# Performance work log

Hardware: AMD Instinct MI355X
Metric: run time of the kernel (lower is better)

## Reference

```python
import jax, jax.numpy as jnp
from jax import lax
import numpy as np

NF = 64   # nf
T = 7     # in_nc == 2*radius+1 frames
KS = 3    # deform kernel size
K = KS * KS


def conv2d(x, w, b, stride=1, pad=1):
    out = lax.conv_general_dilated(x, w, (stride, stride), [(pad, pad), (pad, pad)],
                                   dimension_numbers=('NCHW', 'OIHW', 'NCHW'))
    return out + b[None, :, None, None]


def convT2d(x, w, b):
    # torch ConvTranspose2d(k=4, stride=2, padding=1); w: (Cin, Cout, 4, 4)
    wf = jnp.flip(w, (2, 3)).transpose(1, 0, 2, 3)
    out = lax.conv_general_dilated(x, wf, (1, 1), [(2, 2), (2, 2)], lhs_dilation=(2, 2),
                                   dimension_numbers=('NCHW', 'OIHW', 'NCHW'))
    return out + b[None, :, None, None]


def bilinear_gather(img, ys, xs):
    # img: (C, H, W); ys/xs: (...,) absolute pixel coords; zero padding outside
    C, H, W = img.shape
    y0 = jnp.floor(ys); x0 = jnp.floor(xs)
    wy = ys - y0; wx = xs - x0

    def tap(yi, xi, wgt):
        valid = (yi >= 0) & (yi <= H - 1) & (xi >= 0) & (xi <= W - 1)
        yc = jnp.clip(yi, 0, H - 1).astype(jnp.int32)
        xc = jnp.clip(xi, 0, W - 1).astype(jnp.int32)
        return img[:, yc, xc] * (wgt * valid.astype(img.dtype))

    return (tap(y0, x0, (1 - wy) * (1 - wx)) + tap(y0, x0 + 1, (1 - wy) * wx)
            + tap(y0 + 1, x0, wy * (1 - wx)) + tap(y0 + 1, x0 + 1, wy * wx))


def flow_warp(x, flow):
    # x: (C, H, W); flow: (H, W, 2) with (dx, dy); align_corners=True grid_sample
    # with the normalization in the torch code reduces to absolute-pixel bilinear.
    H, W = x.shape[-2:]
    gy, gx = jnp.meshgrid(jnp.arange(H, dtype=x.dtype), jnp.arange(W, dtype=x.dtype), indexing='ij')
    return bilinear_gather(x, gy + flow[..., 1], gx + flow[..., 0])


def mod_deform_conv(x, off, msk, w, b):
    # Modulated deformable conv v2; deformable_groups = Cin (1 channel per group).
    B, Cin, H, W = x.shape
    G = Cin
    off = off.reshape(B, G, K, 2, H, W)   # per-group (dy, dx) per kernel tap
    msk = msk.reshape(B, G, K, H, W)
    gy, gx = jnp.meshgrid(jnp.arange(H, dtype=x.dtype), jnp.arange(W, dtype=x.dtype), indexing='ij')
    kk = jnp.arange(K)
    ky = (kk // KS - KS // 2).astype(x.dtype)
    kx = (kk % KS - KS // 2).astype(x.dtype)
    ys = gy[None, None, None] + ky[None, None, :, None, None] + off[:, :, :, 0]  # (B,G,K,H,W)
    xs = gx[None, None, None] + kx[None, None, :, None, None] + off[:, :, :, 1]
    xg = x.reshape(B, G, 1, H, W)
    samp = jax.vmap(jax.vmap(jax.vmap(bilinear_gather, in_axes=(None, 0, 0)),
                             in_axes=(0, 0, 0)), in_axes=(0, 0, 0))(xg, ys, xs)
    # samp: (B, G, K, 1, H, W)
    mod = samp * msk[:, :, :, None]
    wk = w.reshape(w.shape[0], G, 1, K)   # (O, G, Cpg=1, K)
    out = jnp.einsum('bgkchw,ogck->bohw', mod, wk)
    return out + b[None, :, None, None]


def _agg(feats, aligned, pred, ff_w, ff_b, dn1_w, dn1_b, dn2_w, dn2_b,
         tr_cw, tr_cb, tr_tw, tr_tb, up1_cw, up1_cb, up1_tw, up1_tb,
         up2_cw, up2_cb, up2_tw, up2_tb):
    B, T_, C, H, W = feats.shape
    ref = feats[:, T_ // 2][:, None]                      # center frame embedding
    p1 = jax.nn.sigmoid(aligned * ref)
    p2 = jax.nn.sigmoid(pred * ref)
    a1 = (aligned * p1).reshape(B, T_ * C, H, W)
    a2 = (pred * p2).reshape(B, T_ * C, H, W)
    f = feats.reshape(B, T_ * C, H, W)
    fuse = lambda z: jax.nn.leaky_relu(conv2d(z, ff_w, ff_b), 0.1)
    out0 = 0.1 * fuse(a1 + a2) + fuse(f)
    out1 = jax.nn.relu(conv2d(out0, dn1_w, dn1_b, stride=2))
    out2 = jax.nn.relu(conv2d(out1, dn2_w, dn2_b, stride=2))
    out = jax.nn.relu(convT2d(jax.nn.relu(conv2d(out2, tr_cw, tr_cb, stride=2)), tr_tw, tr_tb))
    out = jax.nn.relu(convT2d(jax.nn.relu(conv2d(jnp.concatenate([out, out2], 1), up2_cw, up2_cb)), up2_tw, up2_tb))
    out = jax.nn.relu(convT2d(jax.nn.relu(conv2d(jnp.concatenate([out, out1], 1), up1_cw, up1_cb)), up1_tw, up1_tb))
    return out


def _forward(lqs, preds, mv, bw1, bb1, bw2, bb2, dn1_w, dn1_b, dn2_w, dn2_b,
             up1_cw, up1_cb, up1_tw, up1_tb, up2_cw, up2_cb, up2_tw, up2_tb,
             tr_cw, tr_cb, tr_tw, tr_tb, ff_w, ff_b, om_w, om_b, dc_w, dc_b):
    B, T_, H, W = lqs.shape
    bb = lambda z: conv2d(conv2d(z, bw1, bb1), bw2, bb2)
    feat = bb(lqs.reshape(B * T_, 1, H, W)).reshape(B, T_, NF, H, W)
    pred_feat = bb(preds).reshape(B, T_, NF, H, W)
    # alg_MV_fea[:,0] = feat[:,0]; alg_MV_fea[:,i] = warp(feat[:,i-1], mv[:,i-1])
    prev = feat[:, :T_ - 1].reshape(B * (T_ - 1), NF, H, W)
    flows = mv.reshape(B * (T_ - 1), H, W, 2)
    warped = jax.vmap(flow_warp)(prev, flows).reshape(B, T_ - 1, NF, H, W)
    alg = jnp.concatenate([feat[:, :1], warped], axis=1)
    feat_f = _agg(feat, alg, pred_feat, ff_w, ff_b, dn1_w, dn1_b, dn2_w, dn2_b,
                  tr_cw, tr_cb, tr_tw, tr_tb, up1_cw, up1_cb, up1_tw, up1_tb,
                  up2_cw, up2_cb, up2_tw, up2_tb)
    off_msk = conv2d(feat_f, om_w, om_b)      # (B, T*3*K, H, W)
    n_off = T_ * 2 * K
    off = off_msk[:, :n_off]
    m = jax.nn.sigmoid(off_msk[:, n_off:])
    return jax.nn.relu(mod_deform_conv(lqs, off, m, dc_w, dc_b))


def setup_inputs():
    key = jax.random.key(0)
    ks = iter(jax.random.split(key, 40))
    B, H, W = 1, 192, 192
    r = lambda shape: jax.random.normal(next(ks), shape, jnp.float32)
    w = lambda shape: r(shape) * 0.05
    return {
        'lqs': r((B, T, H, W)),
        'preds': r((B * T, 1, H, W)),
        'mv': r((B, T - 1, H, W, 2)),
        'bw1': w((NF, 1, 3, 3)), 'bb1': w((NF,)),
        'bw2': w((NF, NF, 3, 3)), 'bb2': w((NF,)),
        'dn1_w': w((NF, NF, 3, 3)), 'dn1_b': w((NF,)),
        'dn2_w': w((NF, NF, 3, 3)), 'dn2_b': w((NF,)),
        'up1_cw': w((NF, 2 * NF, 3, 3)), 'up1_cb': w((NF,)),
        'up1_tw': w((NF, NF, 4, 4)), 'up1_tb': w((NF,)),
        'up2_cw': w((NF, 2 * NF, 3, 3)), 'up2_cb': w((NF,)),
        'up2_tw': w((NF, NF, 4, 4)), 'up2_tb': w((NF,)),
        'tr_cw': w((NF, NF, 3, 3)), 'tr_cb': w((NF,)),
        'tr_tw': w((NF, NF, 4, 4)), 'tr_tb': w((NF,)),
        'ff_w': w((NF, T * NF, 3, 3)), 'ff_b': w((NF,)),
        'om_w': w((T * 3 * K, NF, 3, 3)), 'om_b': w((T * 3 * K,)),
        'dc_w': w((NF, T, 3, 3)), 'dc_b': w((NF,)),
    }


def reference(lqs, preds, mv, bw1, bb1, bw2, bb2, dn1_w, dn1_b, dn2_w, dn2_b,
              up1_cw, up1_cb, up1_tw, up1_tb, up2_cw, up2_cb, up2_tw, up2_tb,
              tr_cw, tr_cb, tr_tw, tr_tb, ff_w, ff_b, om_w, om_b, dc_w, dc_b):
    return _forward(lqs, preds, mv, bw1, bb1, bw2, bb2, dn1_w, dn1_b, dn2_w, dn2_b,
                    up1_cw, up1_cb, up1_tw, up1_tb, up2_cw, up2_cb, up2_tw, up2_tb,
                    tr_cw, tr_cb, tr_tw, tr_tb, ff_w, ff_b, om_w, om_b, dc_w, dc_b)
```

## Files before the change

### kernel.cpp

```cpp
#include <hip/hip_runtime.h>
#include <math.h>

#define IMH 192
#define IMW 192
#define HWF 36864
#define PDIM 194

typedef unsigned short u16t;
typedef __attribute__((ext_vector_type(8))) short short8;
typedef __attribute__((ext_vector_type(4))) float f32x4;

__device__ __forceinline__ float sigmoidf(float x){ return 1.f/(1.f+expf(-x)); }
__device__ __forceinline__ float lrelu(float x){ return x > 0.f ? x : 0.1f*x; }
__device__ __forceinline__ float b2f(u16t h){ unsigned u = ((unsigned)h)<<16; return __uint_as_float(u); }
__device__ __forceinline__ u16t f2b(float f){
  unsigned u = __float_as_uint(f);
  u += 0x7FFFu + ((u>>16)&1u);
  return (u16t)(u>>16);
}

__device__ __forceinline__ float bilin(const float* __restrict__ img, float ys, float xs, int H, int W){
  float y0f = floorf(ys), x0f = floorf(xs);
  float wy = ys - y0f, wx = xs - x0f;
  int y0 = (int)y0f, x0 = (int)x0f;
  float acc = 0.f;
  #pragma unroll
  for (int dy=0; dy<2; ++dy){
    int yi = y0+dy;
    float wyv = dy ? wy : 1.f-wy;
    if (yi < 0 || yi >= H) continue;
    #pragma unroll
    for (int dx=0; dx<2; ++dx){
      int xi = x0+dx;
      float wxv = dx ? wx : 1.f-wx;
      if (xi < 0 || xi >= W) continue;
      acc += img[yi*W+xi]*(wyv*wxv);
    }
  }
  return acc;
}

struct PkD { const float* w; u16t* dst; int Cin, Cout, NT, total; };
struct PkD8 { PkD d[8]; };
__global__ __launch_bounds__(256) void pack_all(PkD8 ds){
  PkD d = ds.d[blockIdx.y];
  int id = blockIdx.x*256 + threadIdx.x;
  if (id >= d.total) return;
  int j = id & 7, l = (id>>3) & 63;
  int r = id >> 9;
  int nt = r % d.NT; r /= d.NT;
  int KC = d.Cin >> 5;
  int kc = r % KC; int tap = r / KC;
  int c = kc*32 + ((l>>4)<<3) + j;
  int o = nt*16 + (l&15);
  float v = (o < d.Cout) ? d.w[((size_t)o*d.Cin + c)*9 + tap] : 0.f;
  d.dst[id] = f2b(v);
}

struct RpD { const float* w; float* wp; };
struct RpD3 { RpD d[3]; };
__global__ __launch_bounds__(256) void repack_all(RpD3 ds){
  RpD d = ds.d[blockIdx.y];
  int id = blockIdx.x*256 + threadIdx.x;
  int par = id >> 12, o = (id >> 6) & 63, i = id & 63;
  int ry = par >> 1, rx = par & 1;
  #pragma unroll
  for (int jy = 0; jy < 2; ++jy)
    #pragma unroll
    for (int jx = 0; jx < 2; ++jx){
      int ka = 3 - ry - 2*jy, kb = 3 - rx - 2*jx;
      d.wp[((size_t)((par*64 + o)*64 + i))*4 + jy*2 + jx] = d.w[((size_t)(i*64 + o))*16 + ka*4 + kb];
    }
}

struct PzD { u16t* buf; int C, dim, nimg; size_t stride; };
struct PzD5 { PzD d[5]; };
__global__ __launch_bounds__(256) void padzero_all(PzD5 ds){
  PzD d = ds.d[blockIdx.y];
  int per = (4*d.dim - 4)*d.C;
  long total = (long)per*d.nimg;
  for (long id = (long)blockIdx.x*256 + threadIdx.x; id < total; id += (long)gridDim.x*256){
    int n = (int)(id / per), c2 = (int)(id % per);
    int cell = c2 / d.C, c = c2 % d.C;
    int d2 = d.dim - 1;
    int r, col;
    if (cell < d.dim){ r = 0; col = cell; }
    else if (cell < 2*d.dim){ r = d2; col = cell - d.dim; }
    else if (cell < 3*d.dim - 2){ r = cell - 2*d.dim + 1; col = 0; }
    else { r = cell - (3*d.dim - 2) + 1; col = d2; }
    d.buf[(size_t)n*d.stride + ((size_t)r*d.dim + col)*d.C + c] = 0;
  }
}

__global__ __launch_bounds__(256) void padzero2(u16t* buf, int C, int dim){
  int total = (4*dim - 4)*C;
  for (int id = blockIdx.x*256 + threadIdx.x; id < total; id += gridDim.x*256){
    int cell = id / C, c = id % C;
    int d2 = dim - 1;
    int r, col;
    if (cell < dim){ r = 0; col = cell; }
    else if (cell < 2*dim){ r = d2; col = cell - dim; }
    else if (cell < 3*dim - 2){ r = cell - 2*dim + 1; col = 0; }
    else { r = cell - (3*dim - 2) + 1; col = d2; }
    buf[((size_t)r*dim + col)*C + c] = 0;
  }
}

__global__ __launch_bounds__(256) void bbfused(
    const float* __restrict__ lqs, const float* __restrict__ preds,
    const float* __restrict__ w1, const float* __restrict__ b1,
    const u16t* __restrict__ Bp, const float* __restrict__ b2,
    u16t* __restrict__ fpad, u16t* __restrict__ prednhwc)
{
  __shared__ float sIn1[8][20];
  __shared__ float sw1[576];
  __shared__ float sb1[64];
  __shared__ u16t sA[108*68];
  int bid = blockIdx.x;
  bid = (bid & 7)*(gridDim.x >> 3) + (bid >> 3);
  const int tid = threadIdx.x;
  const int img = bid / 576;
  const int rem = bid - img*576;
  const int y0 = (rem/12)*4, xs = (rem%12)*16;
  for (int i = tid; i < 576; i += 256) sw1[i] = w1[i];
  if (tid < 64) sb1[tid] = b1[tid];
  const float* ip = (img < 7) ? (lqs + (size_t)img*HWF) : (preds + (size_t)(img-7)*HWF);
  for (int u = tid; u < 160; u += 256){
    int lr = u/20, lc = u%20;
    int iy = y0 - 2 + lr, ix = xs - 2 + lc;
    sIn1[lr][lc] = (iy >= 0 && iy < IMH && ix >= 0 && ix < IMW) ? ip[iy*IMW + ix] : 0.f;
  }
  __syncthreads();
  for (int u = tid; u < 216; u += 256){
    int px = u >> 1, half = u & 1;
    int rr = px/18, cc = px%18;
    int pr = y0 + rr, pc = xs + cc;
    bool border = (pr == 0) | (pr == 193) | (pc == 0) | (pc == 193);
    float t[9];
    #pragma unroll
    for (int dy = 0; dy < 3; ++dy)
      #pragma unroll
      for (int dx = 0; dx < 3; ++dx) t[dy*3+dx] = sIn1[rr+dy][cc+dx];
    #pragma unroll
    for (int o8 = 0; o8 < 4; ++o8){
      int ob = half*32 + o8*8;
      short8 ov;
      #pragma unroll
      for (int j = 0; j < 8; ++j){
        int o = ob + j;
        float acc = sb1[o];
        #pragma unroll
        for (int k = 0; k < 9; ++k) acc += t[k]*sw1[o*9+k];
        ov[j] = (short)(border ? (u16t)0 : f2b(acc));
      }
      *(short8*)&sA[(size_t)px*68 + ob] = ov;
    }
  }
  __syncthreads();
  const int wave = tid >> 6, lane = tid & 63;
  const int m = lane & 15, q = lane >> 4;
  const int rp = wave >> 1, np = wave & 1;
  f32x4 acc[2][2];
  #pragma unroll
  for (int r = 0; r < 2; ++r)
    #pragma unroll
    for (int n = 0; n < 2; ++n) acc[r][n] = (f32x4){0.f,0.f,0.f,0.f};
  #pragma unroll
  for (int kc = 0; kc < 2; ++kc){
    #pragma unroll
    for (int tap = 0; tap < 9; ++tap){
      const int dy = tap/3, dx = tap%3;
      short8 af[2];
      #pragma unroll
      for (int r = 0; r < 2; ++r)
        af[r] = *(const short8*)&sA[(size_t)((2*rp + r + dy)*18 + dx + m)*68 + kc*32 + q*8];
      const u16t* bp = Bp + ((size_t)(tap*2 + kc)*4 + np*2)*512 + lane*8;
      short8 b0 = *(const short8*)bp;
      short8 b1v = *(const short8*)(bp + 512);
      #pragma unroll
      for (int r = 0; r < 2; ++r){
        acc[r][0] = __builtin_amdgcn_mfma_f32_16x16x32_bf16(af[r], b0, acc[r][0], 0, 0, 0);
        acc[r][1] = __builtin_amdgcn_mfma_f32_16x16x32_bf16(af[r], b1v, acc[r][1], 0, 0, 0);
      }
    }
  }
  const int px0 = q*4;
  #pragma unroll
  for (int r = 0; r < 2; ++r){
    int yout = y0 + 2*rp + r;
    #pragma unroll
    for (int n = 0; n < 2; ++n){
      int oL = (np*2 + n)*16 + m;
      float bv = b2[oL];
      #pragma unroll
      for (int g = 0; g < 4; ++g){
        int px = xs + px0 + g;
        float v = acc[r][n][g] + bv;
        if (img < 7)
          fpad[((size_t)(yout+1)*PDIM + px+1)*448 + (size_t)img*64 + oL] = f2b(v);
        else
          prednhwc[(size_t)(img-7)*((size_t)HWF*64) + ((size_t)yout*IMW + px)*64 + oL] = f2b(v);
      }
    }
  }
}

template<int STREAMS, int KC, int OMODE, int NTT, int SWZ>
__global__ __launch_bounds__(256) void cgemm(
    const u16t* __restrict__ A0, const u16t* __restrict__ A1,
    const u16t* __restrict__ Bp, const float* __restrict__ bias,
    float* __restrict__ outf, u16t* __restrict__ outb, u16t* __restrict__ outb2,
    int Cout, int blocksPerImg, int pitchIn, int csIn, size_t aImgStride, int KCtot)
{
  __shared__ u16t sA[STREAMS*108*40];
  int bid = blockIdx.x;
  if (SWZ) bid = (bid & 7)*(gridDim.x >> 3) + (bid >> 3);
  const int tid = threadIdx.x;
  const int wave = tid >> 6, lane = tid & 63;
  const int m = lane & 15, q = lane >> 4;
  const int img = bid / blocksPerImg;
  const int rem = bid - img*blocksPerImg;
  const int y0 = (rem/12)*4, xs = (rem%12)*16;
  const int rp = wave >> 1, np = wave & 1;
  const int ntB = (OMODE == 5) ? blockIdx.y*4 : 0;
  f32x4 acc[STREAMS][2][2];
  #pragma unroll
  for (int s = 0; s < STREAMS; ++s)
    #pragma unroll
    for (int r = 0; r < 2; ++r)
      #pragma unroll
      for (int n = 0; n < 2; ++n) acc[s][r][n] = (f32x4){0.f,0.f,0.f,0.f};

  #pragma unroll 1
  for (int kc = 0; kc < KC; ++kc){
    if (kc) __syncthreads();
    for (int u = tid; u < STREAMS*216; u += 256){
      int st = u/216, r2 = u%216, p = r2>>1, h = r2&1;
      int rr = p/18, cc = p%18;
      size_t ga = (size_t)img*aImgStride + ((size_t)(y0+rr)*pitchIn + xs+cc)*csIn + kc*32 + h*16;
      const u16t* gp = ((STREAMS==2 && st==1) ? A1 : A0) + ga;
      short8 v0 = *(const short8*)gp;
      short8 v1 = *(const short8*)(gp + 8);
      u16t* lp = &sA[((size_t)(st*108 + p))*40 + h*16];
      *(short8*)lp = v0;
      *(short8*)(lp+8) = v1;
    }
    __syncthreads();
    #pragma unroll
    for (int tap = 0; tap < 9; ++tap){
      const int dy = tap/3, dx = tap%3;
      short8 af[STREAMS][2];
      #pragma unroll
      for (int st = 0; st < STREAMS; ++st)
        #pragma unroll
        for (int r = 0; r < 2; ++r)
          af[st][r] = *(const short8*)&sA[((size_t)(st*108 + (2*rp + r + dy)*18 + dx + m))*40 + q*8];
      const u16t* bp = Bp + ((size_t)(tap*KCtot + kc)*NTT + ntB + np*2)*512 + lane*8;
      short8 b0 = *(const short8*)bp;
      short8 b1 = *(const short8*)(bp + 512);
      #pragma unroll
      for (int st = 0; st < STREAMS; ++st)
        #pragma unroll
        for (int r = 0; r < 2; ++r){
          acc[st][r][0] = __builtin_amdgcn_mfma_f32_16x16x32_bf16(af[st][r], b0, acc[st][r][0], 0, 0, 0);
          acc[st][r][1] = __builtin_amdgcn_mfma_f32_16x16x32_bf16(af[st][r], b1, acc[st][r][1], 0, 0, 0);
        }
    }
  }
  const int px0 = q*4;
  #pragma unroll
  for (int r = 0; r < 2; ++r){
    int yout = y0 + 2*rp + r;
    #pragma unroll
    for (int n = 0; n < 2; ++n){
      int oL = (np*2 + n)*16 + m;
      if (OMODE == 4){
        float bv = bias[oL];
        #pragma unroll
        for (int g = 0; g < 4; ++g){
          int px = xs + px0 + g;
          float v = 0.1f*lrelu(acc[0][r][n][g] + bv) + lrelu(acc[1][r][n][g] + bv);
          outb[((size_t)(yout+1)*PDIM + px+1)*64 + oL] = f2b(v);
        }
      } else {
        int o = ntB*16 + oL;
        if (o < Cout){
          float bv = bias[o];
          #pragma unroll
          for (int g = 0; g < 4; ++g){
            int px = xs + px0 + g;
            outf[(size_t)o*HWF + (size_t)yout*IMW + px] = acc[0][r][n][g] + bv;
          }
        }
      }
    }
  }
}

template<int NT, int KC, int STRIDE, int OMODE, int ACT, int SWZ>
__global__ __launch_bounds__(256) void gconv3(
    const u16t* __restrict__ A0, const u16t* __restrict__ Bp, const float* __restrict__ bias,
    float* __restrict__ outf, u16t* __restrict__ outb,
    int Cout, int Wout, int strips, int blocksPerImg,
    int pitchIn, int csIn, int coIn, size_t aImgStride,
    size_t outImgStride, int pitchOut, int csOut, int coOut,
    int KCtot, int NTtot)
{
  int bid = blockIdx.x;
  if (SWZ) bid = (bid & 7)*(gridDim.x >> 3) + (bid >> 3);
  const int wave = threadIdx.x >> 6;
  const int lane = threadIdx.x & 63;
  const int img = bid / blocksPerImg;
  const int sid = (bid - img*blocksPerImg)*4 + wave;
  const int y = sid / strips, xs = (sid % strips) * 16;
  const int m = lane & 15, q = lane >> 4;
  const int ntOff = blockIdx.y*NT;
  f32x4 acc[NT];
  #pragma unroll
  for (int nt = 0; nt < NT; ++nt) acc[nt] = (f32x4){0.f,0.f,0.f,0.f};

  for (int tap = 0; tap < 9; ++tap){
    int dy = tap/3, dx = tap%3;
    int row = STRIDE*y + dy;
    int col = (STRIDE == 1) ? (xs + m + dx) : (2*(xs + m) + dx);
    size_t abase = (size_t)img*aImgStride + ((size_t)row*pitchIn + col)*csIn + coIn + q*8;
    const u16t* ap0 = A0 + abase;
    const u16t* bp = Bp + ((size_t)(tap*KCtot)*NTtot + ntOff)*512 + lane*8;
    #pragma unroll
    for (int kc = 0; kc < KC; ++kc){
      short8 av0 = *(const short8*)(ap0 + kc*32);
      #pragma unroll
      for (int nt = 0; nt < NT; ++nt){
        short8 bv = *(const short8*)(bp + (size_t)(kc*NTtot + nt)*512);
        acc[nt] = __builtin_amdgcn_mfma_f32_16x16x32_bf16(av0, bv, acc[nt], 0, 0, 0);
      }
    }
  }
  const int prow0 = q*4;
  #pragma unroll
  for (int nt = 0; nt < NT; ++nt){
    int o = (ntOff + nt)*16 + m;
    if (o >= Cout) continue;
    float bv = bias[o];
    #pragma unroll
    for (int r = 0; r < 4; ++r){
      int px = xs + prow0 + r;
      if (px >= Wout) continue;
      float v = acc[nt][r] + bv;
      if (ACT) v = fmaxf(v, 0.f);
      if (OMODE == 0){
        outf[((size_t)img*Cout + o)*((size_t)Wout*Wout) + (size_t)y*Wout + px] = v;
      } else if (OMODE == 1){
        outb[(size_t)img*outImgStride + ((size_t)(y+1)*pitchOut + px+1)*csOut + coOut + o] = f2b(v);
      } else {
        outb[(size_t)img*outImgStride + ((size_t)y*pitchOut + px)*csOut + coOut + o] = f2b(v);
      }
    }
  }
}

__global__ __launch_bounds__(256) void gate_nhwc(
    const u16t* __restrict__ fpad, const u16t* __restrict__ pred,
    const float* __restrict__ mv, u16t* __restrict__ spad)
{
  int bid = blockIdx.x;
  int xcd = bid & 7, lb = bid >> 3;
  int idx = (xcd*18 + lb)*256 + threadIdx.x;
  int y = idx/IMW, x = idx%IMW;
  size_t pc = ((size_t)(y+1)*PDIM + (x+1))*448;
  const u16t* rp = fpad + pc + 192;
  short8 r8[8];
  #pragma unroll
  for (int c8 = 0; c8 < 8; ++c8) r8[c8] = *(const short8*)(rp + c8*8);
  #pragma unroll 1
  for (int t = 0; t < 7; ++t){
    const u16t* pp = pred + ((size_t)t*HWF + idx)*64;
    u16t* sp = spad + pc + (size_t)t*64;
    const u16t* tp[4]; float tw[4];
    if (t == 0){
      tp[0] = fpad + pc; tw[0] = 1.f;
      tp[1] = tp[2] = tp[3] = fpad + pc; tw[1] = tw[2] = tw[3] = 0.f;
    } else {
      float fx = mv[(((size_t)(t-1)*HWF + idx))*2 + 0];
      float fy = mv[(((size_t)(t-1)*HWF + idx))*2 + 1];
      float ys = (float)y + fy, xsf = (float)x + fx;
      float y0f = floorf(ys), x0f = floorf(xsf);
      float wy = ys - y0f, wx = xsf - x0f;
      int y0 = (int)y0f, x0i = (int)x0f;
      int kk = 0;
      #pragma unroll
      for (int dy2 = 0; dy2 < 2; ++dy2)
        #pragma unroll
        for (int dx2 = 0; dx2 < 2; ++dx2){
          int yi = y0+dy2, xi = x0i+dx2;
          float wv = (dy2 ? wy : 1.f-wy)*(dx2 ? wx : 1.f-wx);
          bool ok = (yi >= 0 && yi <= 191 && xi >= 0 && xi <= 191);
          int yc = min(max(yi,0),191), xc = min(max(xi,0),191);
          tp[kk] = fpad + ((size_t)(yc+1)*PDIM + xc+1)*448 + (size_t)(t-1)*64;
          tw[kk] = ok ? wv : 0.f;
          ++kk;
        }
    }
    #pragma unroll
    for (int c8 = 0; c8 < 8; ++c8){
      short8 pv = *(const short8*)(pp + c8*8);
      short8 t0v = *(const short8*)(tp[0] + c8*8);
      short8 t1v = *(const short8*)(tp[1] + c8*8);
      short8 t2v = *(const short8*)(tp[2] + c8*8);
      short8 t3v = *(const short8*)(tp[3] + c8*8);
      short8 ov;
      #pragma unroll
      for (int j = 0; j < 8; ++j){
        float r = b2f((u16t)r8[c8][j]);
        float p = b2f((u16t)pv[j]);
        float a = tw[0]*b2f((u16t)t0v[j]) + tw[1]*b2f((u16t)t1v[j])
                + tw[2]*b2f((u16t)t2v[j]) + tw[3]*b2f((u16t)t3v[j]);
        float sv = a*sigmoidf(a*r) + p*sigmoidf(p*r);
        ov[j] = (short)f2b(sv);
      }
      *(short8*)(sp + c8*8) = ov;
    }
  }
}

__global__ __launch_bounds__(256) void convT_tile2(
    const float* __restrict__ in, const float* __restrict__ wp,
    const float* __restrict__ bias, u16t* __restrict__ outb,
    int Hin, int tilesX, int pitchOut, int csOut, int coOut)
{
  const int CC = 4;
  __shared__ float sIn[CC][10*11];
  __shared__ float sW[16][CC][4][4];
  const int Win = Hin;
  const int o0 = blockIdx.x*16;
  const int tile = blockIdx.y;
  const int ty0 = (tile/tilesX)*16, tx0 = (tile%tilesX)*16;
  const int tid = threadIdx.x;
  const int py = tid>>4, px = tid&15;
  const int ry = py&1, rx = px&1, par = ry*2 + rx;
  const int lr = py>>1, lc = px>>1;
  const int r0 = ty0>>1, c0 = tx0>>1;
  float acc[16] = {};
  for (int ib = 0; ib < 64; ib += CC){
    for (int i = tid; i < CC*100; i += 256){
      int c = i/100, rem = i%100, r = rem/10, col = rem%10;
      int gy = r0 - 1 + r, gx = c0 - 1 + col;
      float v = 0.f;
      if (gy >= 0 && gy < Hin && gx >= 0 && gx < Win)
        v = in[(size_t)(ib + c)*Hin*Win + gy*Win + gx];
      sIn[c][r*11 + col] = v;
    }
    for (int i = tid; i < 1024; i += 256){
      int ol = i >> 6, rem = i & 63, ci = rem >> 4, p2 = (rem >> 2) & 3, j = rem & 3;
      sW[ol][ci][p2][j] = wp[((size_t)((p2*64 + o0 + ol)*64) + ib + ci)*4 + j];
    }
    __syncthreads();
    #pragma unroll
    for (int ci = 0; ci < CC; ++ci){
      int rb = lr + ry, cb = lc + rx;
      float t00 = sIn[ci][rb*11 + cb],     t01 = sIn[ci][rb*11 + cb + 1];
      float t10 = sIn[ci][(rb+1)*11 + cb], t11 = sIn[ci][(rb+1)*11 + cb + 1];
      #pragma unroll
      for (int ol = 0; ol < 16; ++ol){
        const float* wv = &sW[ol][ci][par][0];
        acc[ol] += t00*wv[0] + t01*wv[1] + t10*wv[2] + t11*wv[3];
      }
    }
    __syncthreads();
  }
  int gy = ty0 + py, gx = tx0 + px;
  u16t* op = outb + ((size_t)(gy+1)*pitchOut + gx+1)*csOut + coOut + o0;
  short8 pa, pb;
  #pragma unroll
  for (int i = 0; i < 8; ++i) pa[i] = (short)f2b(fmaxf(acc[i] + bias[o0+i], 0.f));
  #pragma unroll
  for (int i = 0; i < 8; ++i) pb[i] = (short)f2b(fmaxf(acc[8+i] + bias[o0+8+i], 0.f));
  *(short8*)op = pa;
  *(short8*)(op + 8) = pb;
}

__global__ __launch_bounds__(256) void deform_sample_k(
    const float* __restrict__ lqs, const float* __restrict__ om,
    float* __restrict__ vbuf)
{
  int idx = blockIdx.x*256 + threadIdx.x;
  int g = blockIdx.y;
  int h = idx / IMW, x = idx % IMW;
  const float* img = lqs + (size_t)g*HWF;
  #pragma unroll
  for (int k = 0; k < 9; ++k){
    int j = g*9 + k;
    float offy = om[(size_t)(j*2 + 0)*HWF + idx];
    float offx = om[(size_t)(j*2 + 1)*HWF + idx];
    float m = sigmoidf(om[(size_t)(126 + j)*HWF + idx]);
    float ys = (float)(h + (k/3) - 1) + offy;
    float xs = (float)(x + (k%3) - 1) + offx;
    vbuf[(size_t)j*HWF + idx] = bilin(img, ys, xs, IMH, IMW) * m;
  }
}

__global__ __launch_bounds__(256) void deform_out_k(
    const float* __restrict__ vbuf, const float* __restrict__ dcw,
    const float* __restrict__ dcb, float* __restrict__ out)
{
  __shared__ float sw[16*63];
  int idx = blockIdx.x*256 + threadIdx.x;
  int o0 = blockIdx.y*16;
  for (int i = threadIdx.x; i < 16*63; i += 256)
    sw[i] = dcw[(size_t)o0*63 + i];
  __syncthreads();
  float v[63];
  #pragma unroll
  for (int j = 0; j < 63; ++j) v[j] = vbuf[(size_t)j*HWF + idx];
  for (int ol = 0; ol < 16; ++ol){
    float acc = dcb[o0 + ol];
    #pragma unroll
    for (int j = 0; j < 63; ++j) acc += v[j]*sw[ol*63 + j];
    out[(size_t)(o0 + ol)*HWF + idx] = fmaxf(acc, 0.f);
  }
}

extern "C" void kernel_launch(void* const* d_in, const int* in_sizes, int n_in,
                              void* d_out, int out_size, void* d_ws, size_t ws_size,
                              hipStream_t stream)
{
  const float* lqs   = (const float*)d_in[0];
  const float* preds = (const float*)d_in[1];
  const float* mv    = (const float*)d_in[2];
  const float* bw1   = (const float*)d_in[3];
  const float* bb1   = (const float*)d_in[4];
  const float* bw2   = (const float*)d_in[5];
  const float* bb2   = (const float*)d_in[6];
  const float* dn1w  = (const float*)d_in[7];
  const float* dn1b  = (const float*)d_in[8];
  const float* dn2w  = (const float*)d_in[9];
  const float* dn2b  = (const float*)d_in[10];
  const float* up1cw = (const float*)d_in[11];
  const float* up1cb = (const float*)d_in[12];
  const float* up1tw = (const float*)d_in[13];
  const float* up1tb = (const float*)d_in[14];
  const float* up2cw = (const float*)d_in[15];
  const float* up2cb = (const float*)d_in[16];
  const float* up2tw = (const float*)d_in[17];
  const float* up2tb = (const float*)d_in[18];
  const float* trcw  = (const float*)d_in[19];
  const float* trcb  = (const float*)d_in[20];
  const float* trtw  = (const float*)d_in[21];
  const float* trtb  = (const float*)d_in[22];
  const float* ffw   = (const float*)d_in[23];
  const float* ffb   = (const float*)d_in[24];
  const float* omw   = (const float*)d_in[25];
  const float* omb   = (const float*)d_in[26];
  const float* dcw   = (const float*)d_in[27];
  const float* dcb   = (const float*)d_in[28];
  float* outp = (float*)d_out;

  char* p = (char*)d_ws;
  const size_t PIMG64 = (size_t)PDIM*PDIM*64;
  u16t* spadreg  = (u16t*)p; p += 14*PIMG64*2;
  u16t* fpad     = (u16t*)p; p += (size_t)PDIM*PDIM*448*2;
  u16t* prednhwc = (u16t*)p; p += (size_t)7*HWF*64*2;
  u16t* out0pad  = (u16t*)p; p += (size_t)PDIM*PDIM*64*2;
  u16t* cat1pad  = (u16t*)p; p += (size_t)98*98*128*2;
  u16t* cat2pad  = (u16t*)p; p += (size_t)50*50*128*2;
  float* t0      = (float*)p; p += (size_t)24*24*64*4;
  float* u2      = (float*)p; p += (size_t)48*48*64*4;
  float* u1      = (float*)p; p += (size_t)96*96*64*4;
  u16t* ffwpack  = (u16t*)p; p += 258048*2;
  u16t* c2pack   = (u16t*)p; p += 36864*2;
  u16t* ompack   = (u16t*)p; p += 110592*2;
  u16t* dn1pack  = (u16t*)p; p += 36864*2;
  u16t* dn2pack  = (u16t*)p; p += 36864*2;
  u16t* trcpack  = (u16t*)p; p += 36864*2;
  u16t* up2cpack = (u16t*)p; p += 73728*2;
  u16t* up1cpack = (u16t*)p; p += 73728*2;
  float* wp0     = (float*)p; p += 65536*4;
  float* wp1     = (float*)p; p += 65536*4;
  float* wp2     = (float*)p; p += 65536*4;

  u16t* spad = spadreg;
  u16t* featfpad = spadreg;
  float* om = (float*)prednhwc;
  float* vbuf = (float*)fpad;

  dim3 blk(256);
  PkD8 pk = {{ {ffw, ffwpack, 448, 64, 4, 258048}, {bw2, c2pack, 64, 64, 4, 36864},
               {omw, ompack, 64, 189, 12, 110592}, {dn1w, dn1pack, 64, 64, 4, 36864},
               {dn2w, dn2pack, 64, 64, 4, 36864},  {trcw, trcpack, 64, 64, 4, 36864},
               {up2cw, up2cpack, 128, 64, 4, 73728}, {up1cw, up1cpack, 128, 64, 4, 73728} }};
  pack_all<<<dim3(1008,8), blk, 0, stream>>>(pk);
  RpD3 rp3 = {{ {trtw, wp0}, {up2tw, wp1}, {up1tw, wp2} }};
  repack_all<<<dim3(64,3), blk, 0, stream>>>(rp3);
  PzD5 pz = {{ {spad, 448, PDIM, 1, 0}, {fpad, 448, PDIM, 1, 0},
               {out0pad, 64, PDIM, 1, 0}, {cat1pad, 128, 98, 1, 0}, {cat2pad, 128, 50, 1, 0} }};
  padzero_all<<<dim3(2704,5), blk, 0, stream>>>(pz);
  bbfused<<<dim3(8064), blk, 0, stream>>>(lqs, preds, bw1, bb1, c2pack, bb2, fpad, prednhwc);
  gate_nhwc<<<dim3(144), blk, 0, stream>>>(fpad, prednhwc, mv, spad);
  cgemm<2,14,4,4,1><<<dim3(576,1), blk, 0, stream>>>(spad, fpad, ffwpack, ffb,
      nullptr, out0pad, nullptr, 64, 576, PDIM, 448, 0, 14);
  gconv3<1,2,2,1,1,1><<<dim3(144,4), blk, 0, stream>>>(out0pad, dn1pack, dn1b, nullptr, cat1pad,
      64, 96, 6, 144, PDIM, 64, 0, 0, 0, 98, 128, 64, 2, 4);
  gconv3<1,2,2,1,1,0><<<dim3(36,4), blk, 0, stream>>>(cat1pad, dn2pack, dn2b, nullptr, cat2pad,
      64, 48, 3, 36, 98, 128, 64, 0, 0, 50, 128, 64, 2, 4);
  gconv3<1,2,2,0,1,0><<<dim3(12,4), blk, 0, stream>>>(cat2pad, trcpack, trcb, t0, nullptr,
      64, 24, 2, 12, 50, 128, 64, 0, 0, 0, 0, 0, 2, 4);
  convT_tile2<<<dim3(4,9), blk, 0, stream>>>(t0, wp0, trtb, cat2pad, 24, 3, 50, 128, 0);
  gconv3<1,4,1,0,1,0><<<dim3(36,4), blk, 0, stream>>>(cat2pad, up2cpack, up2cb, u2, nullptr,
      64, 48, 3, 36, 50, 128, 0, 0, 0, 0, 0, 0, 4, 4);
  convT_tile2<<<dim3(4,36), blk, 0, stream>>>(u2, wp1, up2tb, cat1pad, 48, 6, 98, 128, 0);
  gconv3<1,4,1,0,1,1><<<dim3(144,4), blk, 0, stream>>>(cat1pad, up1cpack, up1cb, u1, nullptr,
      64, 96, 6, 144, 98, 128, 0, 0, 0, 0, 0, 0, 4, 4);
  padzero2<<<dim3(194), blk, 0, stream>>>(featfpad, 64, PDIM);
  convT_tile2<<<dim3(4,144), blk, 0, stream>>>(u1, wp2, up1tb, featfpad, 96, 12, PDIM, 64, 0);
  cgemm<1,2,5,12,1><<<dim3(576,3), blk, 0, stream>>>(featfpad, nullptr, ompack, omb,
      om, nullptr, nullptr, 189, 576, PDIM, 64, 0, 2);
  deform_sample_k<<<dim3(144,7), blk, 0, stream>>>(lqs, om, vbuf);
  deform_out_k<<<dim3(144,4), blk, 0, stream>>>(vbuf, dcw, dcb, outp);
}
```

Baseline: 604.7 us.

## Compute first backbone conv with MFMA and XOR-swizzle LDS tiles instead of padding

The first 1-to-64 channel 3x3 conv in the fused backbone kernel now runs as a K=9 (zero-padded to 32) bf16 MFMA, using a small prepacked weight buffer, instead of scalar FMAs over shared-memory weights. The backbone and generic conv GEMM kernels also drop their padded LDS row pitch (68/40) in favour of an XOR-style chunk swizzle (64/32 pitch), which shrinks shared memory and is meant to avoid bank conflicts. This adds a tiny packing kernel launch. The first conv now rounds its input to bf16, which changes numerics slightly.

New measurement: 632.8 us. +4.6%, slower.

```diff
diff --git a/kernel.cpp b/kernel.cpp
--- a/kernel.cpp
+++ b/kernel.cpp
@@ -55,6 +55,15 @@
   int o = nt*16 + (l&15);
   float v = (o < d.Cout) ? d.w[((size_t)o*d.Cin + c)*9 + tap] : 0.f;
   d.dst[id] = f2b(v);
+}
+
+__global__ __launch_bounds__(256) void pack_w1(const float* __restrict__ w1, u16t* __restrict__ dst){
+  int id = blockIdx.x*256 + threadIdx.x;
+  int j = id & 7, l = (id>>3) & 63, nt = id >> 9;
+  int o = nt*16 + (l&15);
+  int k = ((l>>4)<<3) + j;
+  float v = (k < 9) ? w1[o*9 + k] : 0.f;
+  dst[id] = f2b(v);
 }
 
 struct RpD { const float* w; float* wp; };
@@ -108,22 +117,18 @@
 
 __global__ __launch_bounds__(256) void bbfused(
     const float* __restrict__ lqs, const float* __restrict__ preds,
-    const float* __restrict__ w1, const float* __restrict__ b1,
+    const u16t* __restrict__ w1pack, const float* __restrict__ b1,
     const u16t* __restrict__ Bp, const float* __restrict__ b2,
     u16t* __restrict__ fpad, u16t* __restrict__ prednhwc)
 {
   __shared__ float sIn1[8][20];
-  __shared__ float sw1[576];
-  __shared__ float sb1[64];
-  __shared__ u16t sA[108*68];
+  __shared__ u16t sA[108*64];
   int bid = blockIdx.x;
   bid = (bid & 7)*(gridDim.x >> 3) + (bid >> 3);
   const int tid = threadIdx.x;
   const int img = bid / 576;
   const int rem = bid - img*576;
   const int y0 = (rem/12)*4, xs = (rem%12)*16;
-  for (int i = tid; i < 576; i += 256) sw1[i] = w1[i];
-  if (tid < 64) sb1[tid] = b1[tid];
   const float* ip = (img < 7) ? (lqs + (size_t)img*HWF) : (preds + (size_t)(img-7)*HWF);
   for (int u = tid; u < 160; u += 256){
     int lr = u/20, lc = u%20;
@@ -131,34 +136,45 @@
     sIn1[lr][lc] = (iy >= 0 && iy < IMH && ix >= 0 && ix < IMW) ? ip[iy*IMW + ix] : 0.f;
   }
   __syncthreads();
-  for (int u = tid; u < 216; u += 256){
-    int px = u >> 1, half = u & 1;
-    int rr = px/18, cc = px%18;
-    int pr = y0 + rr, pc = xs + cc;
-    bool border = (pr == 0) | (pr == 193) | (pc == 0) | (pc == 193);
-    float t[9];
-    #pragma unroll
-    for (int dy = 0; dy < 3; ++dy)
-      #pragma unroll
-      for (int dx = 0; dx < 3; ++dx) t[dy*3+dx] = sIn1[rr+dy][cc+dx];
-    #pragma unroll
-    for (int o8 = 0; o8 < 4; ++o8){
-      int ob = half*32 + o8*8;
-      short8 ov;
-      #pragma unroll
-      for (int j = 0; j < 8; ++j){
-        int o = ob + j;
-        float acc = sb1[o];
-        #pragma unroll
-        for (int k = 0; k < 9; ++k) acc += t[k]*sw1[o*9+k];
-        ov[j] = (short)(border ? (u16t)0 : f2b(acc));
-      }
-      *(short8*)&sA[(size_t)px*68 + ob] = ov;
-    }
-  }
-  __syncthreads();
   const int wave = tid >> 6, lane = tid & 63;
   const int m = lane & 15, q = lane >> 4;
+  short8 bfr = *(const short8*)(w1pack + (size_t)wave*512 + lane*8);
+  f32x4 c1[7];
+  #pragma unroll
+  for (int p = 0; p < 7; ++p){
+    int px = p*16 + m;
+    bool valid = px < 108;
+    int rr = valid ? px/18 : 0, cc = valid ? px%18 : 0;
+    short8 av = {0,0,0,0,0,0,0,0};
+    #pragma unroll
+    for (int j = 0; j < 8; ++j){
+      int k = q*8 + j;
+      if (valid && k < 9){
+        av[j] = (short)f2b(sIn1[rr + k/3][cc + k%3]);
+      }
+    }
+    f32x4 z = {0.f,0.f,0.f,0.f};
+    c1[p] = __builtin_amdgcn_mfma_f32_16x16x32_bf16(av, bfr, z, 0, 0, 0);
+  }
+  {
+    int o = wave*16 + m;
+    float b1v = b1[o];
+    int g = o >> 3, ol = o & 7;
+    #pragma unroll
+    for (int p = 0; p < 7; ++p){
+      #pragma unroll
+      for (int r = 0; r < 4; ++r){
+        int pxo = p*16 + q*4 + r;
+        if (pxo >= 108) continue;
+        int rr2 = pxo/18, cc2 = pxo%18;
+        int pr = y0 + rr2, pc = xs + cc2;
+        bool border = (pr == 0) | (pr == 193) | (pc == 0) | (pc == 193);
+        float v = c1[p][r] + b1v;
+        sA[(size_t)pxo*64 + ((g + pxo)&7)*8 + ol] = border ? (u16t)0 : f2b(v);
+      }
+    }
+  }
+  __syncthreads();
   const int rp = wave >> 1, np = wave & 1;
   f32x4 acc[2][2];
   #pragma unroll
@@ -172,8 +188,10 @@
       const int dy = tap/3, dx = tap%3;
       short8 af[2];
       #pragma unroll
-      for (int r = 0; r < 2; ++r)
-        af[r] = *(const short8*)&sA[(size_t)((2*rp + r + dy)*18 + dx + m)*68 + kc*32 + q*8];
+      for (int r = 0; r < 2; ++r){
+        int px = (2*rp + r + dy)*18 + dx + m;
+        af[r] = *(const short8*)&sA[(size_t)px*64 + ((kc*4 + q + px)&7)*8];
+      }
       const u16t* bp = Bp + ((size_t)(tap*2 + kc)*4 + np*2)*512 + lane*8;
       short8 b0 = *(const short8*)bp;
       short8 b1v = *(const short8*)(bp + 512);
@@ -212,7 +230,7 @@
     float* __restrict__ outf, u16t* __restrict__ outb, u16t* __restrict__ outb2,
     int Cout, int blocksPerImg, int pitchIn, int csIn, size_t aImgStride, int KCtot)
 {
-  __shared__ u16t sA[STREAMS*108*40];
+  __shared__ u16t sA[STREAMS*108*32];
   int bid = blockIdx.x;
   if (SWZ) bid = (bid & 7)*(gridDim.x >> 3) + (bid >> 3);
   const int tid = threadIdx.x;
@@ -241,9 +259,9 @@
       const u16t* gp = ((STREAMS==2 && st==1) ? A1 : A0) + ga;
       short8 v0 = *(const short8*)gp;
       short8 v1 = *(const short8*)(gp + 8);
-      u16t* lp = &sA[((size_t)(st*108 + p))*40 + h*16];
-      *(short8*)lp = v0;
-      *(short8*)(lp+8) = v1;
+      u16t* base = &sA[((size_t)(st*108 + p))*32];
+      *(short8*)(base + ((2*h + p)&3)*8) = v0;
+      *(short8*)(base + ((2*h + 1 + p)&3)*8) = v1;
     }
     __syncthreads();
     #pragma unroll
@@ -253,8 +271,10 @@
       #pragma unroll
       for (int st = 0; st < STREAMS; ++st)
         #pragma unroll
-        for (int r = 0; r < 2; ++r)
-          af[st][r] = *(const short8*)&sA[((size_t)(st*108 + (2*rp + r + dy)*18 + dx + m))*40 + q*8];
+        for (int r = 0; r < 2; ++r){
+          int px = (2*rp + r + dy)*18 + dx + m;
+          af[st][r] = *(const short8*)&sA[((size_t)(st*108 + px))*32 + ((q + px)&3)*8];
+        }
       const u16t* bp = Bp + ((size_t)(tap*KCtot + kc)*NTT + ntB + np*2)*512 + lane*8;
       short8 b0 = *(const short8*)bp;
       short8 b1 = *(const short8*)(bp + 512);
@@ -574,6 +594,7 @@
   u16t* trcpack  = (u16t*)p; p += 36864*2;
   u16t* up2cpack = (u16t*)p; p += 73728*2;
   u16t* up1cpack = (u16t*)p; p += 73728*2;
+  u16t* w1pack   = (u16t*)p; p += 2048*2;
   float* wp0     = (float*)p; p += 65536*4;
   float* wp1     = (float*)p; p += 65536*4;
   float* wp2     = (float*)p; p += 65536*4;
@@ -589,12 +610,13 @@
                {dn2w, dn2pack, 64, 64, 4, 36864},  {trcw, trcpack, 64, 64, 4, 36864},
                {up2cw, up2cpack, 128, 64, 4, 73728}, {up1cw, up1cpack, 128, 64, 4, 73728} }};
   pack_all<<<dim3(1008,8), blk, 0, stream>>>(pk);
+  pack_w1<<<dim3(8), blk, 0, stream>>>(bw1, w1pack);
   RpD3 rp3 = {{ {trtw, wp0}, {up2tw, wp1}, {up1tw, wp2} }};
   repack_all<<<dim3(64,3), blk, 0, stream>>>(rp3);
   PzD5 pz = {{ {spad, 448, PDIM, 1, 0}, {fpad, 448, PDIM, 1, 0},
                {out0pad, 64, PDIM, 1, 0}, {cat1pad, 128, 98, 1, 0}, {cat2pad, 128, 50, 1, 0} }};
   padzero_all<<<dim3(2704,5), blk, 0, stream>>>(pz);
-  bbfused<<<dim3(8064), blk, 0, stream>>>(lqs, preds, bw1, bb1, c2pack, bb2, fpad, prednhwc);
+  bbfused<<<dim3(8064), blk, 0, stream>>>(lqs, preds, w1pack, bb1, c2pack, bb2, fpad, prednhwc);
   gate_nhwc<<<dim3(144), blk, 0, stream>>>(fpad, prednhwc, mv, spad);
   cgemm<2,14,4,4,1><<<dim3(576,1), blk, 0, stream>>>(spad, fpad, ffwpack, ffb,
       nullptr, out0pad, nullptr, 64, 576, PDIM, 448, 0, 14);
```

## Swizzle LDS tiles and restructure first-conv as lane-per-channel sliding window

Applied to the files above, without the earlier changes.

Replaces the padded LDS row pitch (68/40) with unpadded rows (64/32) and an XOR-style rotation of the 8-element chunks by pixel index, which keeps bank conflicts low while shrinking shared memory. In bbfused, the first 1-channel 3x3 conv is reorganized so each lane owns one output channel with its weights held in registers, and each wave walks a run of pixels reusing a sliding 3x3 input window. This removes the shared weight arrays and the redundant input reloads, at the cost of a serial 27-iteration loop per wave and scalar 16-bit LDS stores.

Measured after the change: 614.6 us. About the same (+1.6%).

```diff
diff --git a/kernel.cpp b/kernel.cpp
--- a/kernel.cpp
+++ b/kernel.cpp
@@ -113,51 +113,53 @@
     u16t* __restrict__ fpad, u16t* __restrict__ prednhwc)
 {
   __shared__ float sIn1[8][20];
-  __shared__ float sw1[576];
-  __shared__ float sb1[64];
-  __shared__ u16t sA[108*68];
+  __shared__ u16t sA[108*64];
   int bid = blockIdx.x;
   bid = (bid & 7)*(gridDim.x >> 3) + (bid >> 3);
   const int tid = threadIdx.x;
   const int img = bid / 576;
   const int rem = bid - img*576;
   const int y0 = (rem/12)*4, xs = (rem%12)*16;
-  for (int i = tid; i < 576; i += 256) sw1[i] = w1[i];
-  if (tid < 64) sb1[tid] = b1[tid];
   const float* ip = (img < 7) ? (lqs + (size_t)img*HWF) : (preds + (size_t)(img-7)*HWF);
   for (int u = tid; u < 160; u += 256){
     int lr = u/20, lc = u%20;
     int iy = y0 - 2 + lr, ix = xs - 2 + lc;
     sIn1[lr][lc] = (iy >= 0 && iy < IMH && ix >= 0 && ix < IMW) ? ip[iy*IMW + ix] : 0.f;
   }
+  const int wave = tid >> 6, lane = tid & 63;
+  float wr[9];
+  #pragma unroll
+  for (int k = 0; k < 9; ++k) wr[k] = w1[lane*9 + k];
+  float b1v = b1[lane];
+  const int gsw = lane >> 3, ol = lane & 7;
   __syncthreads();
-  for (int u = tid; u < 216; u += 256){
-    int px = u >> 1, half = u & 1;
-    int rr = px/18, cc = px%18;
-    int pr = y0 + rr, pc = xs + cc;
-    bool border = (pr == 0) | (pr == 193) | (pc == 0) | (pc == 193);
+  {
     float t[9];
-    #pragma unroll
-    for (int dy = 0; dy < 3; ++dy)
-      #pragma unroll
-      for (int dx = 0; dx < 3; ++dx) t[dy*3+dx] = sIn1[rr+dy][cc+dx];
-    #pragma unroll
-    for (int o8 = 0; o8 < 4; ++o8){
-      int ob = half*32 + o8*8;
-      short8 ov;
-      #pragma unroll
-      for (int j = 0; j < 8; ++j){
-        int o = ob + j;
-        float acc = sb1[o];
+    #pragma unroll 1
+    for (int i = 0; i < 27; ++i){
+      int px = wave*27 + i;
+      int rr = px/18, cc = px%18;
+      if (i == 0 || cc == 0){
         #pragma unroll
-        for (int k = 0; k < 9; ++k) acc += t[k]*sw1[o*9+k];
-        ov[j] = (short)(border ? (u16t)0 : f2b(acc));
-      }
-      *(short8*)&sA[(size_t)px*68 + ob] = ov;
+        for (int dy = 0; dy < 3; ++dy)
+          #pragma unroll
+          for (int dx = 0; dx < 3; ++dx) t[dy*3+dx] = sIn1[rr+dy][cc+dx];
+      } else {
+        #pragma unroll
+        for (int dy = 0; dy < 3; ++dy){
+          t[dy*3] = t[dy*3+1]; t[dy*3+1] = t[dy*3+2];
+          t[dy*3+2] = sIn1[rr+dy][cc+2];
+        }
+      }
+      float acc = b1v;
+      #pragma unroll
+      for (int k = 0; k < 9; ++k) acc += t[k]*wr[k];
+      int pr = y0 + rr, pc = xs + cc;
+      bool border = (pr == 0) | (pr == 193) | (pc == 0) | (pc == 193);
+      sA[(size_t)px*64 + ((gsw + px)&7)*8 + ol] = border ? (u16t)0 : f2b(acc);
     }
   }
   __syncthreads();
-  const int wave = tid >> 6, lane = tid & 63;
   const int m = lane & 15, q = lane >> 4;
   const int rp = wave >> 1, np = wave & 1;
   f32x4 acc[2][2];
@@ -172,15 +174,17 @@
       const int dy = tap/3, dx = tap%3;
       short8 af[2];
       #pragma unroll
-      for (int r = 0; r < 2; ++r)
-        af[r] = *(const short8*)&sA[(size_t)((2*rp + r + dy)*18 + dx + m)*68 + kc*32 + q*8];
+      for (int r = 0; r < 2; ++r){
+        int px = (2*rp + r + dy)*18 + dx + m;
+        af[r] = *(const short8*)&sA[(size_t)px*64 + ((kc*4 + q + px)&7)*8];
+      }
       const u16t* bp = Bp + ((size_t)(tap*2 + kc)*4 + np*2)*512 + lane*8;
       short8 b0 = *(const short8*)bp;
-      short8 b1v = *(const short8*)(bp + 512);
+      short8 b1w = *(const short8*)(bp + 512);
       #pragma unroll
       for (int r = 0; r < 2; ++r){
         acc[r][0] = __builtin_amdgcn_mfma_f32_16x16x32_bf16(af[r], b0, acc[r][0], 0, 0, 0);
-        acc[r][1] = __builtin_amdgcn_mfma_f32_16x16x32_bf16(af[r], b1v, acc[r][1], 0, 0, 0);
+        acc[r][1] = __builtin_amdgcn_mfma_f32_16x16x32_bf16(af[r], b1w, acc[r][1], 0, 0, 0);
       }
     }
   }
@@ -212,7 +216,7 @@
     float* __restrict__ outf, u16t* __restrict__ outb, u16t* __restrict__ outb2,
     int Cout, int blocksPerImg, int pitchIn, int csIn, size_t aImgStride, int KCtot)
 {
-  __shared__ u16t sA[STREAMS*108*40];
+  __shared__ u16t sA[STREAMS*108*32];
   int bid = blockIdx.x;
   if (SWZ) bid = (bid & 7)*(gridDim.x >> 3) + (bid >> 3);
   const int tid = threadIdx.x;
@@ -241,9 +245,9 @@
       const u16t* gp = ((STREAMS==2 && st==1) ? A1 : A0) + ga;
       short8 v0 = *(const short8*)gp;
       short8 v1 = *(const short8*)(gp + 8);
-      u16t* lp = &sA[((size_t)(st*108 + p))*40 + h*16];
-      *(short8*)lp = v0;
-      *(short8*)(lp+8) = v1;
+      u16t* base = &sA[((size_t)(st*108 + p))*32];
+      *(short8*)(base + ((2*h + p)&3)*8) = v0;
+      *(short8*)(base + ((2*h + 1 + p)&3)*8) = v1;
     }
     __syncthreads();
     #pragma unroll
@@ -253,8 +257,10 @@
       #pragma unroll
       for (int st = 0; st < STREAMS; ++st)
         #pragma unroll
-        for (int r = 0; r < 2; ++r)
-          af[st][r] = *(const short8*)&sA[((size_t)(st*108 + (2*rp + r + dy)*18 + dx + m))*40 + q*8];
+        for (int r = 0; r < 2; ++r){
+          int px = (2*rp + r + dy)*18 + dx + m;
+          af[st][r] = *(const short8*)&sA[((size_t)(st*108 + px))*32 + ((q + px)&3)*8];
+        }
       const u16t* bp = Bp + ((size_t)(tap*KCtot + kc)*NTT + ntB + np*2)*512 + lane*8;
       short8 b0 = *(const short8*)bp;
       short8 b1 = *(const short8*)(bp + 512);
```
